# Kernel optimization log

Measured on AMD Instinct MI355X. Metric: run time of the kernel, lower is better.

## Reference

```python
import jax, jax.numpy as jnp
import numpy as np

FIX_SIGMA = (1.0, 2.0, 4.0, 8.0, 16.0)


def setup_inputs() -> dict:
    key = jax.random.key(0)
    k1, k2 = jax.random.split(key)
    B, C, D = 512, 32, 512
    source = jax.random.normal(k1, (B, C, D), dtype=jnp.float32)
    target = jax.random.normal(k2, (B, C, D), dtype=jnp.float32)
    return {"source": source, "target": target}


def _mmd(source, target):
    B = source.shape[0]
    total = jnp.concatenate([source, target], axis=0)  # [N, C, D], N = 2B
    # Pairwise per-channel squared L2 distance via norm expansion
    # (mathematically identical to ((x_i - x_j)**2).sum(-1), no [N,N,C,D] intermediate)
    sq = jnp.sum(total * total, axis=-1)  # [N, C]
    cross = jnp.einsum("icd,jcd->ijc", total, total)  # [N, N, C]
    L2 = sq[:, None, :] + sq[None, :, :] - 2.0 * cross  # [N, N, C]
    kernels = sum(jnp.exp(-L2 / sigma) for sigma in FIX_SIGMA)  # [N, N, C]
    XX = kernels[:B, :B, :]
    YY = kernels[B:, B:, :]
    XY = kernels[:B, B:, :]
    YX = kernels[B:, :B, :]
    loss_1 = XX + YY - XY - YX  # [B, B, C]
    # mean over dim0, mean over dim0 again (i.e. both batch dims), sum over channels
    return jnp.sum(jnp.mean(loss_1, axis=(0, 1)))


def reference(source, target):
    return _mmd(source, target)
```

## Files before the change

kernel.cpp:

```cpp
#include <hip/hip_runtime.h>

namespace {

constexpr int kC = 32;
constexpr int kD = 512;
constexpr int kB = 512;
constexpr int kN = 1024;
constexpr int kCD = kC * kD;
constexpr int BM = 128;
constexpr int BKt = 32;
constexpr int KT = kD / BKt;
constexpr int NG = 20;

typedef float f32x4 __attribute__((ext_vector_type(4)));
typedef short s16x8 __attribute__((ext_vector_type(8)));

__device__ __constant__ int gTi[NG] = {0,0,0,0, 1,1,1,1, 2,2,2, 3,3,3, 4,4, 5,5, 6, 7};
__device__ __constant__ int gT0[NG] = {0,2,4,6, 1,3,5,7, 2,4,6, 3,5,7, 4,6, 5,7, 6, 7};
__device__ __constant__ int gT1[NG] = {1,3,5,7, 2,4,6,7, 3,5,7, 4,6,7, 5,7, 6,7, 7, 7};

__device__ inline unsigned int pack_bf16(float a, float b) {
  unsigned int ua = __float_as_uint(a);
  unsigned int ub = __float_as_uint(b);
  ua += 0x7fffu + ((ua >> 16) & 1u);
  ub += 0x7fffu + ((ub >> 16) & 1u);
  return (ua >> 16) | (ub & 0xffff0000u);
}

__global__ void prep_kernel(const float* __restrict__ src,
                            const float* __restrict__ tgt,
                            float* __restrict__ sq,
                            unsigned int* __restrict__ tot,
                            float* __restrict__ out) {
  if (blockIdx.x == 0 && threadIdx.x == 0) *out = 0.f;
  int gw = (blockIdx.x * blockDim.x + threadIdx.x) >> 6;
  int lane = threadIdx.x & 63;
  int i = gw >> 5;
  int c = gw & 31;
  const float* p = (i < kB ? src + (size_t)i * kCD
                           : tgt + (size_t)(i - kB) * kCD) + c * kD;
  f32x4 v0 = *(const f32x4*)(p + lane * 8);
  f32x4 v1 = *(const f32x4*)(p + lane * 8 + 4);

  uint4 w = make_uint4(pack_bf16(v0.x, v0.y), pack_bf16(v0.z, v0.w),
                       pack_bf16(v1.x, v1.y), pack_bf16(v1.z, v1.w));
  *(uint4*)(tot + (size_t)(c * kN + i) * (kD / 2) + lane * 4) = w;

  float s = v0.x * v0.x + v0.y * v0.y + v0.z * v0.z + v0.w * v0.w
          + v1.x * v1.x + v1.y * v1.y + v1.z * v1.z + v1.w * v1.w;
#pragma unroll
  for (int o = 32; o > 0; o >>= 1) s += __shfl_down(s, o);
  if (lane == 0) sq[c * kN + i] = s;
}

__launch_bounds__(512, 2)
__global__ void mmd_kernel(const unsigned short* __restrict__ tot,
                           const float* __restrict__ sq,
                           float* __restrict__ out) {
  const int b = blockIdx.x;
  const int c = b & 31;
  const int g = b >> 5;
  const int ti = gTi[g];
  const int t0 = gT0[g];
  const int t1 = gT1[g];

  __shared__ __align__(16) unsigned short lA[3][BM * BKt];
  __shared__ __align__(16) unsigned short lB[3][2][BM * BKt];
  __shared__ float wsum[8];

  const int t = threadIdx.x;
  const int lane = t & 63;
  const int wid = t >> 6;
  const int bsel = wid >> 2;
  const int wr = (wid >> 1) & 1;
  const int wc = wid & 1;

  const unsigned short* gA  = tot + (size_t)(c * kN + ti * BM) * kD;
  const unsigned short* gB0 = tot + (size_t)(c * kN + t0 * BM) * kD;
  const unsigned short* gB1 = tot + (size_t)(c * kN + t1 * BM) * kD;

  const int srow = ((lane >> 3) << 1) + ((lane >> 2) & 1);
  const int scch = (lane & 3) ^ ((lane >> 3) & 3);

  auto STAGE = [&](int buf, int ks) {
    int r = 16 * wid + srow;
    size_t off = (size_t)r * kD + ks * BKt + scch * 8;
    __builtin_amdgcn_global_load_lds(
        (const __attribute__((address_space(1))) unsigned int*)(gA + off),
        (__attribute__((address_space(3))) unsigned int*)&lA[buf][wid * 512],
        16, 0, 0);
    __builtin_amdgcn_global_load_lds(
        (const __attribute__((address_space(1))) unsigned int*)(gB0 + off),
        (__attribute__((address_space(3))) unsigned int*)&lB[buf][0][wid * 512],
        16, 0, 0);
    __builtin_amdgcn_global_load_lds(
        (const __attribute__((address_space(1))) unsigned int*)(gB1 + off),
        (__attribute__((address_space(3))) unsigned int*)&lB[buf][1][wid * 512],
        16, 0, 0);
  };

  const int l15 = lane & 15;
  const int s4 = lane >> 4;
  const int laneoff = ((l15 >> 1) << 7) + ((l15 & 1) << 6) +
                      ((s4 ^ ((l15 >> 1) & 3)) << 4);

  f32x4 acc[4][4] = {};

  STAGE(0, 0);
  STAGE(1, 1);

#pragma unroll
  for (int ks = 0; ks < KT; ++ks) {
    if (ks + 1 < KT) asm volatile("s_waitcnt vmcnt(3)" ::: "memory");
    else             asm volatile("s_waitcnt vmcnt(0)" ::: "memory");
    __builtin_amdgcn_sched_barrier(0);
    __builtin_amdgcn_s_barrier();

    const int buf = ks % 3;
    const char* Abase = (const char*)lA[buf] + wr * 4096 + laneoff;
    const char* Bbase = (const char*)lB[buf][bsel] + wc * 4096 + laneoff;
    s16x8 aF[4], bF[4];
#pragma unroll
    for (int m = 0; m < 4; ++m) aF[m] = *(const s16x8*)(Abase + m * 1024);
#pragma unroll
    for (int n = 0; n < 4; ++n) bF[n] = *(const s16x8*)(Bbase + n * 1024);

    if (ks + 2 < KT) STAGE((ks + 2) % 3, ks + 2);

    __builtin_amdgcn_s_setprio(1);
#pragma unroll
    for (int m = 0; m < 4; ++m)
#pragma unroll
      for (int n = 0; n < 4; ++n)
        acc[m][n] = __builtin_amdgcn_mfma_f32_16x16x32_bf16(
            aF[m], bF[n], acc[m][n], 0, 0, 0);
    __builtin_amdgcn_s_setprio(0);
  }

  const int tj = bsel ? t1 : t0;
  const float sgn = ((ti < 4) == (tj < 4)) ? 1.f : -1.f;
  const float wgt = ((ti == tj) ? 1.f : 2.f) * ((t0 == t1) ? 0.5f : 1.f);
  const float scale = sgn * wgt / 262144.f;
  const float* sqA = sq + c * kN + ti * BM + wr * 64;
  const float* sqB = sq + c * kN + tj * BM + wc * 64;

  float local = 0.f;
#pragma unroll
  for (int m = 0; m < 4; ++m) {
    float sqa_r[4];
#pragma unroll
    for (int rI = 0; rI < 4; ++rI)
      sqa_r[rI] = sqA[m * 16 + s4 * 4 + rI];
#pragma unroll
    for (int n = 0; n < 4; ++n) {
      float sqb_ = sqB[n * 16 + l15];
#pragma unroll
      for (int rI = 0; rI < 4; ++rI) {
        float L2 = sqa_r[rI] + sqb_ - 2.f * acc[m][n][rI];
        float tt = __expf(L2 * -0.0625f);
        float t2 = tt * tt, t4 = t2 * t2, t8 = t4 * t4;
        local += tt + t2 + t4 + t8 + t8 * t8;
      }
    }
  }
  local *= scale;

#pragma unroll
  for (int o = 32; o > 0; o >>= 1) local += __shfl_down(local, o);
  if (lane == 0) wsum[wid] = local;
  __syncthreads();
  if (t == 0) {
    float s = 0.f;
#pragma unroll
    for (int w = 0; w < 8; ++w) s += wsum[w];
    atomicAdd(out, s);
  }
}

}

extern "C" void kernel_launch(void* const* d_in, const int* in_sizes, int n_in,
                              void* d_out, int out_size, void* d_ws,
                              size_t ws_size, hipStream_t stream) {
  const float* src = (const float*)d_in[0];
  const float* tgt = (const float*)d_in[1];
  float* out = (float*)d_out;

  float* sq = (float*)d_ws;
  unsigned int* tot = (unsigned int*)((char*)d_ws + (size_t)kC * kN * 4);

  {
    int blocks = (kN * kC) / 4;
    prep_kernel<<<blocks, 256, 0, stream>>>(src, tgt, sq, tot, out);
  }
  {
    int blocks = NG * kC;
    mmd_kernel<<<blocks, 512, 0, stream>>>((const unsigned short*)tot, sq, out);
  }
}
```

Before: 55.41 us.

## Use 256x256 upper-triangle tiles with in-tile diagonal masking and double buffering

```diff
diff --git a/kernel.cpp b/kernel.cpp
--- a/kernel.cpp
+++ b/kernel.cpp
@@ -7,17 +7,14 @@
 constexpr int kB = 512;
 constexpr int kN = 1024;
 constexpr int kCD = kC * kD;
-constexpr int BM = 128;
+constexpr int BM = 256;
 constexpr int BKt = 32;
 constexpr int KT = kD / BKt;
-constexpr int NG = 20;
+constexpr int T2 = kN / BM;
+constexpr int NP = T2 * (T2 + 1) / 2;
 
 typedef float f32x4 __attribute__((ext_vector_type(4)));
 typedef short s16x8 __attribute__((ext_vector_type(8)));
-
-__device__ __constant__ int gTi[NG] = {0,0,0,0, 1,1,1,1, 2,2,2, 3,3,3, 4,4, 5,5, 6, 7};
-__device__ __constant__ int gT0[NG] = {0,2,4,6, 1,3,5,7, 2,4,6, 3,5,7, 4,6, 5,7, 6, 7};
-__device__ __constant__ int gT1[NG] = {1,3,5,7, 2,4,6,7, 3,5,7, 4,6,7, 5,7, 6,7, 7, 7};
 
 __device__ inline unsigned int pack_bf16(float a, float b) {
   unsigned int ua = __float_as_uint(a);
@@ -59,44 +56,42 @@
                            float* __restrict__ out) {
   const int b = blockIdx.x;
   const int c = b & 31;
-  const int g = b >> 5;
-  const int ti = gTi[g];
-  const int t0 = gT0[g];
-  const int t1 = gT1[g];
-
-  __shared__ __align__(16) unsigned short lA[3][BM * BKt];
-  __shared__ __align__(16) unsigned short lB[3][2][BM * BKt];
+  int p = b >> 5;
+  int ti = 0;
+  while (p >= T2 - ti) { p -= T2 - ti; ++ti; }
+  const int tj = ti + p;
+
+  __shared__ __align__(16) unsigned short lA[2][BM * BKt];
+  __shared__ __align__(16) unsigned short lB[2][BM * BKt];
   __shared__ float wsum[8];
 
   const int t = threadIdx.x;
   const int lane = t & 63;
   const int wid = t >> 6;
-  const int bsel = wid >> 2;
-  const int wr = (wid >> 1) & 1;
-  const int wc = wid & 1;
-
-  const unsigned short* gA  = tot + (size_t)(c * kN + ti * BM) * kD;
-  const unsigned short* gB0 = tot + (size_t)(c * kN + t0 * BM) * kD;
-  const unsigned short* gB1 = tot + (size_t)(c * kN + t1 * BM) * kD;
+  const int wr = wid >> 2;
+  const int wc = wid & 3;
+
+  const unsigned short* gA = tot + (size_t)(c * kN + ti * BM) * kD;
+  const unsigned short* gB = tot + (size_t)(c * kN + tj * BM) * kD;
 
   const int srow = ((lane >> 3) << 1) + ((lane >> 2) & 1);
   const int scch = (lane & 3) ^ ((lane >> 3) & 3);
 
   auto STAGE = [&](int buf, int ks) {
-    int r = 16 * wid + srow;
-    size_t off = (size_t)r * kD + ks * BKt + scch * 8;
-    __builtin_amdgcn_global_load_lds(
-        (const __attribute__((address_space(1))) unsigned int*)(gA + off),
-        (__attribute__((address_space(3))) unsigned int*)&lA[buf][wid * 512],
-        16, 0, 0);
-    __builtin_amdgcn_global_load_lds(
-        (const __attribute__((address_space(1))) unsigned int*)(gB0 + off),
-        (__attribute__((address_space(3))) unsigned int*)&lB[buf][0][wid * 512],
-        16, 0, 0);
-    __builtin_amdgcn_global_load_lds(
-        (const __attribute__((address_space(1))) unsigned int*)(gB1 + off),
-        (__attribute__((address_space(3))) unsigned int*)&lB[buf][1][wid * 512],
-        16, 0, 0);
+#pragma unroll
+    for (int q = 0; q < 2; ++q) {
+      int seg = wid * 2 + q;
+      int r = 16 * seg + srow;
+      size_t off = (size_t)r * kD + ks * BKt + scch * 8;
+      __builtin_amdgcn_global_load_lds(
+          (const __attribute__((address_space(1))) unsigned int*)(gA + off),
+          (__attribute__((address_space(3))) unsigned int*)&lA[buf][seg * 512],
+          16, 0, 0);
+      __builtin_amdgcn_global_load_lds(
+          (const __attribute__((address_space(1))) unsigned int*)(gB + off),
+          (__attribute__((address_space(3))) unsigned int*)&lB[buf][seg * 512],
+          16, 0, 0);
+    }
   };
 
   const int l15 = lane & 15;
@@ -104,32 +99,30 @@
   const int laneoff = ((l15 >> 1) << 7) + ((l15 & 1) << 6) +
                       ((s4 ^ ((l15 >> 1) & 3)) << 4);
 
-  f32x4 acc[4][4] = {};
+  f32x4 acc[8][4] = {};
 
   STAGE(0, 0);
-  STAGE(1, 1);
 
 #pragma unroll
   for (int ks = 0; ks < KT; ++ks) {
-    if (ks + 1 < KT) asm volatile("s_waitcnt vmcnt(3)" ::: "memory");
-    else             asm volatile("s_waitcnt vmcnt(0)" ::: "memory");
+    asm volatile("s_waitcnt vmcnt(0)" ::: "memory");
     __builtin_amdgcn_sched_barrier(0);
     __builtin_amdgcn_s_barrier();
 
-    const int buf = ks % 3;
-    const char* Abase = (const char*)lA[buf] + wr * 4096 + laneoff;
-    const char* Bbase = (const char*)lB[buf][bsel] + wc * 4096 + laneoff;
-    s16x8 aF[4], bF[4];
-#pragma unroll
-    for (int m = 0; m < 4; ++m) aF[m] = *(const s16x8*)(Abase + m * 1024);
+    const int buf = ks & 1;
+    if (ks + 1 < KT) STAGE(buf ^ 1, ks + 1);
+
+    const char* Abase = (const char*)lA[buf] + wr * 8192 + laneoff;
+    const char* Bbase = (const char*)lB[buf] + wc * 4096 + laneoff;
+    s16x8 aF[8], bF[4];
+#pragma unroll
+    for (int m = 0; m < 8; ++m) aF[m] = *(const s16x8*)(Abase + m * 1024);
 #pragma unroll
     for (int n = 0; n < 4; ++n) bF[n] = *(const s16x8*)(Bbase + n * 1024);
 
-    if (ks + 2 < KT) STAGE((ks + 2) % 3, ks + 2);
-
     __builtin_amdgcn_s_setprio(1);
 #pragma unroll
-    for (int m = 0; m < 4; ++m)
+    for (int m = 0; m < 8; ++m)
 #pragma unroll
       for (int n = 0; n < 4; ++n)
         acc[m][n] = __builtin_amdgcn_mfma_f32_16x16x32_bf16(
@@ -137,16 +130,15 @@
     __builtin_amdgcn_s_setprio(0);
   }
 
-  const int tj = bsel ? t1 : t0;
-  const float sgn = ((ti < 4) == (tj < 4)) ? 1.f : -1.f;
-  const float wgt = ((ti == tj) ? 1.f : 2.f) * ((t0 == t1) ? 0.5f : 1.f);
-  const float scale = sgn * wgt / 262144.f;
-  const float* sqA = sq + c * kN + ti * BM + wr * 64;
+  const float sgn = ((ti < 2) == (tj < 2)) ? 1.f : -1.f;
+  const float scale = sgn / 262144.f;
+  const bool diag = (ti == tj);
+  const float* sqA = sq + c * kN + ti * BM + wr * 128;
   const float* sqB = sq + c * kN + tj * BM + wc * 64;
 
   float local = 0.f;
 #pragma unroll
-  for (int m = 0; m < 4; ++m) {
+  for (int m = 0; m < 8; ++m) {
     float sqa_r[4];
 #pragma unroll
     for (int rI = 0; rI < 4; ++rI)
@@ -159,7 +151,15 @@
         float L2 = sqa_r[rI] + sqb_ - 2.f * acc[m][n][rI];
         float tt = __expf(L2 * -0.0625f);
         float t2 = tt * tt, t4 = t2 * t2, t8 = t4 * t4;
-        local += tt + t2 + t4 + t8 + t8 * t8;
+        float sumt = tt + t2 + t4 + t8 + t8 * t8;
+        if (diag) {
+          int gr = wr * 128 + m * 16 + s4 * 4 + rI;
+          int gc = wc * 64 + n * 16 + l15;
+          float w = gr < gc ? 2.f : (gr == gc ? 1.f : 0.f);
+          local += w * sumt;
+        } else {
+          local += 2.f * sumt;
+        }
       }
     }
   }
@@ -194,7 +194,7 @@
     prep_kernel<<<blocks, 256, 0, stream>>>(src, tgt, sq, tot, out);
   }
   {
-    int blocks = NG * kC;
+    int blocks = NP * kC;
     mmd_kernel<<<blocks, 512, 0, stream>>>((const unsigned short*)tot, sq, out);
   }
 }
```

Measured after the change: 65.97 us. 1.19x slower.
